# Optimization experiments

Measured on AMD Instinct MI355X. Metric: run time of the kernel, lower is better.

The kernel has to match this reference:

```python
import jax, jax.numpy as jnp
import numpy as np

NUM_LEVELS = 4
RADIUS = 4


def setup_inputs() -> dict:
    key = jax.random.key(0)
    k1, k2, k3 = jax.random.split(key, 3)
    B, C, H, W = 2, 256, 64, 64
    N = 4
    fmap1 = jax.random.normal(k1, (B, C, H, W), dtype=jnp.float32)
    fmap2 = jax.random.normal(k2, (B, C, H, W), dtype=jnp.float32)
    # coords channel 0 = x in [0, W-1], channel 1 = y in [0, H-1]
    coords = jax.random.uniform(k3, (B, N, 2, H, W), dtype=jnp.float32) * (W - 1)
    return {"fmap1": fmap1, "fmap2": fmap2, "coords": coords}


def _bilinear_gather(corr, x, y):
    """Zero-padded bilinear sampling (grid_sample align_corners=True semantics).
    corr: (B, P, h2, w2) per-query-pixel correlation maps.
    x, y: (B, N, P, K2) absolute pixel coords into (w2, h2).
    Returns (B, N, P, K2)."""
    Bv, P, h2, w2 = corr.shape
    x0 = jnp.floor(x)
    y0 = jnp.floor(y)
    wx1 = x - x0
    wy1 = y - y0
    b = jnp.arange(Bv)[:, None, None, None]
    p = jnp.arange(P)[None, None, :, None]

    def corner(yi, xi):
        valid = (xi >= 0) & (xi <= w2 - 1) & (yi >= 0) & (yi <= h2 - 1)
        xi_c = jnp.clip(xi, 0, w2 - 1).astype(jnp.int32)
        yi_c = jnp.clip(yi, 0, h2 - 1).astype(jnp.int32)
        v = corr[b, p, yi_c, xi_c]
        return jnp.where(valid, v, jnp.zeros((), corr.dtype))

    v00 = corner(y0, x0)
    v01 = corner(y0, x0 + 1)
    v10 = corner(y0 + 1, x0)
    v11 = corner(y0 + 1, x0 + 1)
    return ((1 - wy1) * (1 - wx1) * v00 + (1 - wy1) * wx1 * v01
            + wy1 * (1 - wx1) * v10 + wy1 * wx1 * v11)


def reference(fmap1, fmap2, coords):
    B, C, H, W = fmap1.shape
    _, N = coords.shape[0], coords.shape[1]
    P = H * W
    r = RADIUS
    K = 2 * r + 1
    K2 = K * K

    # All-pairs correlation: (B, P_query, H2, W2), scaled by 1/sqrt(C) (RAFT)
    f1 = fmap1.reshape(B, C, P)
    f2 = fmap2.reshape(B, C, P)
    corr = jnp.einsum('bcp,bcq->bpq', f1, f2) / jnp.sqrt(jnp.asarray(C, fmap1.dtype))
    corr = corr.reshape(B, P, H, W)

    # Pyramid via 2x2 average pooling (stride 2, no padding)
    pyramid = [corr]
    c = corr
    for _ in range(NUM_LEVELS - 1):
        h2, w2 = c.shape[-2:]
        c = c.reshape(B, P, h2 // 2, 2, w2 // 2, 2).mean(axis=(3, 5))
        pyramid.append(c)

    # Window offsets. Faithful to the torch code: delta = stack(meshgrid(dy, dx, 'ij'))
    # so delta[...,0] = yy is added to the x-channel, delta[...,1] = xx to the y-channel.
    d = jnp.linspace(-r, r, K).astype(coords.dtype)
    yy, xx = jnp.meshgrid(d, d, indexing='ij')
    off_x = yy.reshape(1, 1, 1, K2)  # added to coords[...,0]
    off_y = xx.reshape(1, 1, 1, K2)  # added to coords[...,1]

    cx = coords[:, :, 0].reshape(B, N, P)  # (B, N, P)
    cy = coords[:, :, 1].reshape(B, N, P)

    outs = []
    for i, cl in enumerate(pyramid):
        scale = jnp.asarray(2.0 ** i, coords.dtype)
        x = cx[..., None] / scale + off_x  # (B, N, P, K2)
        y = cy[..., None] / scale + off_y
        v = _bilinear_gather(cl, x, y)     # (B, N, P, K2)
        outs.append(v.reshape(B, N, H, W, K2))

    out = jnp.concatenate(outs, axis=-1)   # (B, N, H, W, L*K2)
    Ctot = out.shape[-1]
    # Matches torch: contiguous (B,N,H,W,C) reshaped row-major to (B, N*C, H, W)
    out = out.reshape(B, N * Ctot, H, W)
    return out.astype(jnp.float32)
```

## Files before the change

### kernel.cpp

```cpp
#include <hip/hip_runtime.h>
#include <hip/hip_bf16.h>
#include <cstdint>

#define B_    2
#define C_    256
#define H_    64
#define W_    64
#define P_    (H_*W_)
#define N_    4
#define RAD   4
#define K2_   81
#define CTOT  (4*K2_)

typedef __bf16 bf16x8 __attribute__((ext_vector_type(8)));
typedef float  f32x4  __attribute__((ext_vector_type(4)));

__device__ __forceinline__ void gload_lds16(const void* g, void* l) {
    __builtin_amdgcn_global_load_lds(
        (const __attribute__((address_space(1))) void*)g,
        (__attribute__((address_space(3))) void*)l,
        16, 0, 0);
}

__global__ void transpose_cvt(const float* __restrict__ in,
                              __hip_bfloat16* __restrict__ out) {
    __shared__ float tile[32][33];
    const int b  = blockIdx.z;
    const int p0 = blockIdx.x * 32;
    const int c0 = blockIdx.y * 32;
    const int tx = threadIdx.x;
    const int ty = threadIdx.y;
    const float* src = in + ((size_t)b * C_ + c0) * P_ + p0;
    #pragma unroll
    for (int i = 0; i < 32; i += 8)
        tile[ty + i][tx] = src[(size_t)(ty + i) * P_ + tx];
    __syncthreads();
    __hip_bfloat16* dst = out + ((size_t)b * P_ + p0) * C_ + c0;
    #pragma unroll
    for (int i = 0; i < 32; i += 8)
        dst[(size_t)(ty + i) * C_ + tx] = __float2bfloat16(tile[tx][ty + i]);
}

#define TSTR 136

__global__ __launch_bounds__(256) void gemm_corr(
    const short* __restrict__ f1t,
    const short* __restrict__ f2t,
    __hip_bfloat16* __restrict__ corr0,
    __hip_bfloat16* __restrict__ corr1)
{
    __shared__ short smem[128 * TSTR];
    short* As = smem;
    short* Bs = smem + 8192;

    const int tid  = threadIdx.x;
    const int lane = tid & 63;
    const int wv   = tid >> 6;
    const int wm   = (wv >> 1) * 64;
    const int wn   = (wv & 1) * 64;
    const int b    = blockIdx.z;
    const int bx   = blockIdx.x;
    const int m0   = blockIdx.y * 128;
    const int n0   = bx * 128;
    const int qd   = lane >> 4;
    const int l15  = lane & 15;

    const short* gA[4];
    const short* gB[4];
    int ldsOff[4];
    #pragma unroll
    for (int it = 0; it < 4; ++it) {
        const int ci = it * 256 + tid;
        const int r  = ci >> 3;
        const int cp = ci & 7;
        const int kc = cp ^ (r & 7);
        gA[it] = f1t + ((size_t)(b * P_ + m0 + r)) * C_ + kc * 8;
        gB[it] = f2t + ((size_t)(b * P_ + n0 + r)) * C_ + kc * 8;
        ldsOff[it] = (it * 256 + wv * 64) * 8;
    }

    int aAddr[4][2], bAddr[4][2];
    #pragma unroll
    for (int i = 0; i < 4; ++i) {
        const int m = wm + i * 16 + l15;
        const int n = wn + i * 16 + l15;
        #pragma unroll
        for (int s = 0; s < 2; ++s) {
            const int lc = s * 4 + qd;
            aAddr[i][s] = m * 64 + ((lc ^ (m & 7)) * 8);
            bAddr[i][s] = n * 64 + ((lc ^ (n & 7)) * 8);
        }
    }

    f32x4 zero = {0.f, 0.f, 0.f, 0.f};
    f32x4 acc[4][4];
    #pragma unroll
    for (int mi = 0; mi < 4; ++mi)
        #pragma unroll
        for (int ni = 0; ni < 4; ++ni)
            acc[mi][ni] = zero;

    for (int kt = 0; kt < 4; ++kt) {
        const int k0 = kt * 64;
        #pragma unroll
        for (int it = 0; it < 4; ++it) {
            gload_lds16(gA[it] + k0, As + ldsOff[it]);
            gload_lds16(gB[it] + k0, Bs + ldsOff[it]);
        }
        __syncthreads();
        #pragma unroll
        for (int s = 0; s < 2; ++s) {
            bf16x8 af[4], bfr[4];
            #pragma unroll
            for (int i = 0; i < 4; ++i) {
                af[i]  = *(const bf16x8*)(As + aAddr[i][s]);
                bfr[i] = *(const bf16x8*)(Bs + bAddr[i][s]);
            }
            #pragma unroll
            for (int mi = 0; mi < 4; ++mi)
                #pragma unroll
                for (int ni = 0; ni < 4; ++ni)
                    acc[mi][ni] = __builtin_amdgcn_mfma_f32_16x16x32_bf16(
                        af[mi], bfr[ni], acc[mi][ni], 0, 0, 0);
        }
        __syncthreads();
    }

    const float sc = 0.0625f;
    __hip_bfloat16* tile = (__hip_bfloat16*)smem;
    #pragma unroll
    for (int mi = 0; mi < 4; ++mi) {
        #pragma unroll
        for (int ni = 0; ni < 4; ++ni) {
            #pragma unroll
            for (int r = 0; r < 4; ++r) {
                const int rl = wm + mi * 16 + qd * 4 + r;
                const int cl = wn + ni * 16 + l15;
                tile[rl * TSTR + cl] = __float2bfloat16(acc[mi][ni][r] * sc);
            }
        }
    }
    __syncthreads();

    #pragma unroll
    for (int i = 0; i < 8; ++i) {
        const int cid = i * 256 + tid;
        const int tr  = cid >> 4;
        const int tc  = cid & 15;
        const float4 v = *(const float4*)(smem + tr * TSTR + tc * 8);
        *(float4*)(corr0 + ((size_t)(b * P_ + m0 + tr)) * P_ + n0 + tc * 8) = v;
    }

    #pragma unroll
    for (int i = 0; i < 16; ++i) {
        const int oid = i * 256 + tid;
        const int pr  = oid >> 5;
        const int pc  = oid & 31;
        const uint32_t u0 = *(const uint32_t*)(smem + pr * TSTR + 2 * pc);
        const uint32_t u1 = *(const uint32_t*)(smem + pr * TSTR + 64 + 2 * pc);
        const float a0 = __uint_as_float(u0 << 16);
        const float a1 = __uint_as_float(u0 & 0xffff0000u);
        const float b0 = __uint_as_float(u1 << 16);
        const float b1 = __uint_as_float(u1 & 0xffff0000u);
        corr1[((size_t)(b * P_ + m0 + pr)) * 1024 + bx * 32 + pc] =
            __float2bfloat16((a0 + a1 + b0 + b1) * 0.25f);
    }
}

__global__ __launch_bounds__(256) void pool23(
    const __hip_bfloat16* __restrict__ c1,
    __hip_bfloat16* __restrict__ c2,
    __hip_bfloat16* __restrict__ c3) {
    __shared__ float sm[256];
    const int bp  = blockIdx.x;
    const int tid = threadIdx.x;
    const int y2 = tid >> 4, x2 = tid & 15;
    const __hip_bfloat16* src = c1 + (size_t)bp * 1024 + (2 * y2) * 32 + 2 * x2;
    const float v = (__bfloat162float(src[0]) + __bfloat162float(src[1]) +
                     __bfloat162float(src[32]) + __bfloat162float(src[33])) * 0.25f;
    c2[(size_t)bp * 256 + tid] = __float2bfloat16(v);
    sm[tid] = v;
    __syncthreads();
    if (tid < 64) {
        const int y3 = tid >> 3, x3 = tid & 7;
        const float* r0 = sm + (2 * y3) * 16 + 2 * x3;
        const float w = (r0[0] + r0[1] + r0[16] + r0[17]) * 0.25f;
        c3[(size_t)bp * 64 + tid] = __float2bfloat16(w);
    }
}

__global__ __launch_bounds__(256) void gather2(
    const float* __restrict__ coords,
    const __hip_bfloat16* __restrict__ c0,
    const __hip_bfloat16* __restrict__ c1,
    const __hip_bfloat16* __restrict__ c2,
    const __hip_bfloat16* __restrict__ c3,
    float* __restrict__ out) {
    __shared__ float patch[4][110];
    const int tid  = threadIdx.x;
    const int lane = tid & 63;
    const int n    = tid >> 6;
    const int bp   = blockIdx.x;
    const int b    = bp >> 12;
    const int p    = bp & (P_ - 1);

    const float cx = coords[((size_t)((b * N_ + n) * 2 + 0)) * P_ + p];
    const float cy = coords[((size_t)((b * N_ + n) * 2 + 1)) * P_ + p];
    float* pw = patch[n];
    const size_t obase = ((size_t)(b * N_ + n) * P_ + p) * CTOT;

    #pragma unroll
    for (int lvl = 0; lvl < 4; ++lvl) {
        const __hip_bfloat16* corr =
            (lvl == 0) ? c0 : (lvl == 1) ? c1 : (lvl == 2) ? c2 : c3;
        const int hw = H_ >> lvl;
        const float inv = 1.0f / (float)(1 << lvl);
        const float x = cx * inv, y = cy * inv;
        const float x0f = floorf(x), y0f = floorf(y);
        const int x0 = (int)x0f, y0 = (int)y0f;
        const float wx = x - x0f, wy = y - y0f;
        const __hip_bfloat16* src = corr + (size_t)(b * P_ + p) * (hw * hw);

        __syncthreads();
        #pragma unroll
        for (int it = 0; it < 2; ++it) {
            const int idx = lane + it * 64;
            if (idx < 100) {
                const int r  = idx / 10;
                const int cc = idx - r * 10;
                const int gr = y0 - RAD + r;
                const int gc = x0 - RAD + cc;
                const bool ok = (gr >= 0) & (gr < hw) & (gc >= 0) & (gc < hw);
                float v = 0.f;
                if (ok) v = __bfloat162float(src[gr * hw + gc]);
                pw[r * 11 + cc] = v;
            }
        }
        __syncthreads();

        const float omy = 1.f - wy, omx = 1.f - wx;
        const float w00 = omy * omx, w01 = omy * wx;
        const float w10 = wy * omx,  w11 = wy * wx;
        #pragma unroll
        for (int it = 0; it < 2; ++it) {
            const int k2 = lane + it * 64;
            if (k2 < K2_) {
                const int ki = k2 / 9;
                const int kj = k2 - ki * 9;
                const float* pr = pw + kj * 11 + ki;
                const float v = w00 * pr[0] + w01 * pr[1] +
                                w10 * pr[11] + w11 * pr[12];
                out[obase + lvl * K2_ + k2] = v;
            }
        }
    }
}

extern "C" void kernel_launch(void* const* d_in, const int* in_sizes, int n_in,
                              void* d_out, int out_size, void* d_ws, size_t ws_size,
                              hipStream_t stream) {
    const float* fmap1  = (const float*)d_in[0];
    const float* fmap2  = (const float*)d_in[1];
    const float* coords = (const float*)d_in[2];
    float* out = (float*)d_out;

    char* ws = (char*)d_ws;
    __hip_bfloat16* f1t = (__hip_bfloat16*)ws;
    __hip_bfloat16* f2t = (__hip_bfloat16*)(ws + 4194304);
    __hip_bfloat16* c0  = (__hip_bfloat16*)(ws + 8388608);
    __hip_bfloat16* c1  = (__hip_bfloat16*)(ws + 75497472);
    __hip_bfloat16* c2  = (__hip_bfloat16*)(ws + 92274688);
    __hip_bfloat16* c3  = (__hip_bfloat16*)(ws + 96468992);

    {
        dim3 grid(P_ / 32, C_ / 32, B_);
        dim3 blk(32, 8);
        transpose_cvt<<<grid, blk, 0, stream>>>(fmap1, f1t);
        transpose_cvt<<<grid, blk, 0, stream>>>(fmap2, f2t);
    }

    {
        dim3 grid(P_ / 128, P_ / 128, B_);
        gemm_corr<<<grid, 256, 0, stream>>>((const short*)f1t, (const short*)f2t,
                                            c0, c1);
    }

    pool23<<<B_ * P_, 256, 0, stream>>>(c1, c2, c3);

    gather2<<<B_ * P_, 256, 0, stream>>>(coords, c0, c1, c2, c3, out);
}
```

Baseline: 133.6 us.

## Fuse pyramid pooling into gather kernel and merge transpose launches

Levels 2 and 3 of the pyramid are now computed in shared memory inside the gather kernel from the level-1 map, so the separate pool kernel and its global writes and reads go away. The gather loads all four level patches in one pass with a single barrier instead of two barriers per level, then writes all 324 outputs per query. The two transpose launches are also merged into one grid. In exchange, every gather block re-reads the full 1024-entry level-1 map for its pixel and does redundant pooling work, with more shared memory per block.

```diff
diff --git a/kernel.cpp b/kernel.cpp
--- a/kernel.cpp
+++ b/kernel.cpp
@@ -22,10 +22,16 @@
         16, 0, 0);
 }
 
-__global__ void transpose_cvt(const float* __restrict__ in,
-                              __hip_bfloat16* __restrict__ out) {
+__global__ void transpose_cvt(const float* __restrict__ in0,
+                              const float* __restrict__ in1,
+                              __hip_bfloat16* __restrict__ out0,
+                              __hip_bfloat16* __restrict__ out1) {
     __shared__ float tile[32][33];
-    const int b  = blockIdx.z;
+    const int z     = blockIdx.z;
+    const int which = z >> 1;
+    const int b     = z & 1;
+    const float* in          = which ? in1  : in0;
+    __hip_bfloat16* out      = which ? out1 : out0;
     const int p0 = blockIdx.x * 32;
     const int c0 = blockIdx.y * 32;
     const int tx = threadIdx.x;
@@ -167,36 +173,15 @@
     }
 }
 
-__global__ __launch_bounds__(256) void pool23(
-    const __hip_bfloat16* __restrict__ c1,
-    __hip_bfloat16* __restrict__ c2,
-    __hip_bfloat16* __restrict__ c3) {
-    __shared__ float sm[256];
-    const int bp  = blockIdx.x;
-    const int tid = threadIdx.x;
-    const int y2 = tid >> 4, x2 = tid & 15;
-    const __hip_bfloat16* src = c1 + (size_t)bp * 1024 + (2 * y2) * 32 + 2 * x2;
-    const float v = (__bfloat162float(src[0]) + __bfloat162float(src[1]) +
-                     __bfloat162float(src[32]) + __bfloat162float(src[33])) * 0.25f;
-    c2[(size_t)bp * 256 + tid] = __float2bfloat16(v);
-    sm[tid] = v;
-    __syncthreads();
-    if (tid < 64) {
-        const int y3 = tid >> 3, x3 = tid & 7;
-        const float* r0 = sm + (2 * y3) * 16 + 2 * x3;
-        const float w = (r0[0] + r0[1] + r0[16] + r0[17]) * 0.25f;
-        c3[(size_t)bp * 64 + tid] = __float2bfloat16(w);
-    }
-}
-
-__global__ __launch_bounds__(256) void gather2(
+#define SEL4(e, a0, a1, a2, a3) ((e)==0?(a0):(e)==1?(a1):(e)==2?(a2):(a3))
+
+__global__ __launch_bounds__(256) void gather3(
     const float* __restrict__ coords,
     const __hip_bfloat16* __restrict__ c0,
     const __hip_bfloat16* __restrict__ c1,
-    const __hip_bfloat16* __restrict__ c2,
-    const __hip_bfloat16* __restrict__ c3,
     float* __restrict__ out) {
-    __shared__ float patch[4][110];
+    __shared__ float pool_sm[320];
+    __shared__ float patch[4][440];
     const int tid  = threadIdx.x;
     const int lane = tid & 63;
     const int n    = tid >> 6;
@@ -204,54 +189,92 @@
     const int b    = bp >> 12;
     const int p    = bp & (P_ - 1);
 
+    const __hip_bfloat16* c0b = c0 + (size_t)bp * 4096;
+    const __hip_bfloat16* c1b = c1 + (size_t)bp * 1024;
+
+    {
+        const int y2 = tid >> 4, x2 = tid & 15;
+        const uint32_t u0 = *(const uint32_t*)(c1b + (2 * y2) * 32 + 2 * x2);
+        const uint32_t u1 = *(const uint32_t*)(c1b + (2 * y2 + 1) * 32 + 2 * x2);
+        const float a0 = __uint_as_float(u0 << 16);
+        const float a1 = __uint_as_float(u0 & 0xffff0000u);
+        const float b0 = __uint_as_float(u1 << 16);
+        const float b1 = __uint_as_float(u1 & 0xffff0000u);
+        pool_sm[tid] = (a0 + a1 + b0 + b1) * 0.25f;
+    }
+    __syncthreads();
+    if (tid < 64) {
+        const int y3 = tid >> 3, x3 = tid & 7;
+        const float* r0 = pool_sm + (2 * y3) * 16 + 2 * x3;
+        pool_sm[256 + tid] = (r0[0] + r0[1] + r0[16] + r0[17]) * 0.25f;
+    }
+    __syncthreads();
+
     const float cx = coords[((size_t)((b * N_ + n) * 2 + 0)) * P_ + p];
     const float cy = coords[((size_t)((b * N_ + n) * 2 + 1)) * P_ + p];
-    float* pw = patch[n];
-    const size_t obase = ((size_t)(b * N_ + n) * P_ + p) * CTOT;
-
-    #pragma unroll
-    for (int lvl = 0; lvl < 4; ++lvl) {
-        const __hip_bfloat16* corr =
-            (lvl == 0) ? c0 : (lvl == 1) ? c1 : (lvl == 2) ? c2 : c3;
-        const int hw = H_ >> lvl;
-        const float inv = 1.0f / (float)(1 << lvl);
+
+    int x0i[4], y0i[4];
+    float w00[4], w01[4], w10[4], w11[4];
+    #pragma unroll
+    for (int l = 0; l < 4; ++l) {
+        const float inv = 1.0f / (float)(1 << l);
         const float x = cx * inv, y = cy * inv;
         const float x0f = floorf(x), y0f = floorf(y);
-        const int x0 = (int)x0f, y0 = (int)y0f;
         const float wx = x - x0f, wy = y - y0f;
-        const __hip_bfloat16* src = corr + (size_t)(b * P_ + p) * (hw * hw);
-
-        __syncthreads();
-        #pragma unroll
-        for (int it = 0; it < 2; ++it) {
-            const int idx = lane + it * 64;
-            if (idx < 100) {
-                const int r  = idx / 10;
-                const int cc = idx - r * 10;
-                const int gr = y0 - RAD + r;
-                const int gc = x0 - RAD + cc;
+        x0i[l] = (int)x0f - RAD;
+        y0i[l] = (int)y0f - RAD;
+        w00[l] = (1.f - wy) * (1.f - wx);
+        w01[l] = (1.f - wy) * wx;
+        w10[l] = wy * (1.f - wx);
+        w11[l] = wy * wx;
+    }
+
+    float* pw = patch[n];
+
+    #pragma unroll
+    for (int it = 0; it < 7; ++it) {
+        const int idx = it * 64 + lane;
+        if (idx < 440) {
+            const int lvl = idx / 110;
+            const int rem = idx - lvl * 110;
+            const int r   = rem / 11;
+            const int cc  = rem - r * 11;
+            if (cc < 10) {
+                const int hw = H_ >> lvl;
+                const int gr = SEL4(lvl, y0i[0], y0i[1], y0i[2], y0i[3]) + r;
+                const int gc = SEL4(lvl, x0i[0], x0i[1], x0i[2], x0i[3]) + cc;
                 const bool ok = (gr >= 0) & (gr < hw) & (gc >= 0) & (gc < hw);
                 float v = 0.f;
-                if (ok) v = __bfloat162float(src[gr * hw + gc]);
-                pw[r * 11 + cc] = v;
+                if (ok) {
+                    if (lvl < 2) {
+                        const __hip_bfloat16* cp = (lvl == 0) ? c0b : c1b;
+                        v = __bfloat162float(cp[gr * hw + gc]);
+                    } else {
+                        const int li = (lvl == 2) ? (gr * 16 + gc)
+                                                  : (256 + gr * 8 + gc);
+                        v = pool_sm[li];
+                    }
+                }
+                pw[idx] = v;
             }
         }
-        __syncthreads();
-
-        const float omy = 1.f - wy, omx = 1.f - wx;
-        const float w00 = omy * omx, w01 = omy * wx;
-        const float w10 = wy * omx,  w11 = wy * wx;
-        #pragma unroll
-        for (int it = 0; it < 2; ++it) {
-            const int k2 = lane + it * 64;
-            if (k2 < K2_) {
-                const int ki = k2 / 9;
-                const int kj = k2 - ki * 9;
-                const float* pr = pw + kj * 11 + ki;
-                const float v = w00 * pr[0] + w01 * pr[1] +
-                                w10 * pr[11] + w11 * pr[12];
-                out[obase + lvl * K2_ + k2] = v;
-            }
+    }
+
+    const size_t obase = ((size_t)(b * N_ + n) * P_ + p) * CTOT;
+    #pragma unroll
+    for (int it = 0; it < 6; ++it) {
+        const int o = it * 64 + lane;
+        if (o < CTOT) {
+            const int lvl = o / K2_;
+            const int k2  = o - lvl * K2_;
+            const int ki  = k2 / 9;
+            const int kj  = k2 - ki * 9;
+            const float* pr = pw + lvl * 110 + kj * 11 + ki;
+            const float a = SEL4(lvl, w00[0], w00[1], w00[2], w00[3]);
+            const float bq = SEL4(lvl, w01[0], w01[1], w01[2], w01[3]);
+            const float c = SEL4(lvl, w10[0], w10[1], w10[2], w10[3]);
+            const float d = SEL4(lvl, w11[0], w11[1], w11[2], w11[3]);
+            out[obase + o] = a * pr[0] + bq * pr[1] + c * pr[11] + d * pr[12];
         }
     }
 }
@@ -269,14 +292,11 @@
     __hip_bfloat16* f2t = (__hip_bfloat16*)(ws + 4194304);
     __hip_bfloat16* c0  = (__hip_bfloat16*)(ws + 8388608);
     __hip_bfloat16* c1  = (__hip_bfloat16*)(ws + 75497472);
-    __hip_bfloat16* c2  = (__hip_bfloat16*)(ws + 92274688);
-    __hip_bfloat16* c3  = (__hip_bfloat16*)(ws + 96468992);
 
     {
-        dim3 grid(P_ / 32, C_ / 32, B_);
+        dim3 grid(P_ / 32, C_ / 32, 2 * B_);
         dim3 blk(32, 8);
-        transpose_cvt<<<grid, blk, 0, stream>>>(fmap1, f1t);
-        transpose_cvt<<<grid, blk, 0, stream>>>(fmap2, f2t);
+        transpose_cvt<<<grid, blk, 0, stream>>>(fmap1, fmap2, f1t, f2t);
     }
 
     {
@@ -285,7 +305,5 @@
                                             c0, c1);
     }
 
-    pool23<<<B_ * P_, 256, 0, stream>>>(c1, c2, c3);
-
-    gather2<<<B_ * P_, 256, 0, stream>>>(coords, c0, c1, c2, c3, out);
-}
+    gather3<<<B_ * P_, 256, 0, stream>>>(coords, c0, c1, out);
+}
```

Result: faster. 127.0 us (-4.9%).
